# Kernel tuning notes

Hardware: AMD Instinct MI355X
Metric: run time of the kernel (lower is better)

## Reference

```python
import jax, jax.numpy as jnp
import numpy as np

N_UNI = 32; N_G = 4; N_PPG = 8
MAX_D = 100.0; MIN_D = 0.5
SOM_SIGMA = 2.0; G_STD = 2.5
ORIG = jnp.array([-25.6, -25.6, -2.0], jnp.float32); VS = 0.4
NZ = 16; GW = 128; GL = 128; DIM = 128
H_IMG = 352; W_IMG = 1216

def pe(x):
    # positional encoding: num_freqs=6, include_input -> 3 + 36 = 39 dims
    f = 2.0 ** jnp.arange(6, dtype=x.dtype)
    xf = x[..., None] * f  # (...,3,6)
    s = x.shape[:-1]
    return jnp.concatenate([x, jnp.sin(xf).reshape(s + (18,)), jnp.cos(xf).reshape(s + (18,))], axis=-1)

def resnet_fc(z, x, P):
    # pixelNeRF-style ResnetFC with latent injection per block
    w_in, b_in, wz, bz, w0, b0, w1, b1, w_out, b_out = P
    h = x @ w_in + b_in
    for i in range(3):
        h = h + z @ wz[i] + bz[i]
        net = jax.nn.relu(h) @ w0[i] + b0[i]
        h = h + jax.nn.relu(net) @ w1[i] + b1[i]
    return jax.nn.relu(h) @ w_out + b_out

def trilinear(grid, pts):
    # grid: (NZ,GW,GL,DIM); pts: (N,3) lidar coords -> trilinear gather, 0 outside
    g = (pts - ORIG) / VS
    gx, gy, gz = g[:, 0], g[:, 1], g[:, 2]
    inb = (gx >= 0) & (gx <= GW - 1) & (gy >= 0) & (gy <= GL - 1) & (gz >= 0) & (gz <= NZ - 1)
    gx = jnp.clip(gx, 0.0, GW - 1.0); gy = jnp.clip(gy, 0.0, GL - 1.0); gz = jnp.clip(gz, 0.0, NZ - 1.0)
    x0 = jnp.clip(jnp.floor(gx).astype(jnp.int32), 0, GW - 2)
    y0 = jnp.clip(jnp.floor(gy).astype(jnp.int32), 0, GL - 2)
    z0 = jnp.clip(jnp.floor(gz).astype(jnp.int32), 0, NZ - 2)
    fx = gx - x0; fy = gy - y0; fz = gz - z0
    def c(zi, xi, yi, w):
        return grid[zi, xi, yi] * w[:, None]
    feat = (c(z0, x0, y0, (1 - fz) * (1 - fx) * (1 - fy)) + c(z0, x0, y0 + 1, (1 - fz) * (1 - fx) * fy)
            + c(z0, x0 + 1, y0, (1 - fz) * fx * (1 - fy)) + c(z0, x0 + 1, y0 + 1, (1 - fz) * fx * fy)
            + c(z0 + 1, x0, y0, fz * (1 - fx) * (1 - fy)) + c(z0 + 1, x0, y0 + 1, fz * (1 - fx) * fy)
            + c(z0 + 1, x0 + 1, y0, fz * fx * (1 - fy)) + c(z0 + 1, x0 + 1, y0 + 1, fz * fx * fy))
    return feat * inb[:, None].astype(feat.dtype)

def bilinear(img, uv):
    # img: (3,H,W); uv: (N,2) (u=col, v=row) -> (N,3)
    _, H, W = img.shape
    u = jnp.clip(uv[:, 0], 0.0, W - 1.0); v = jnp.clip(uv[:, 1], 0.0, H - 1.0)
    u0 = jnp.clip(jnp.floor(u).astype(jnp.int32), 0, W - 2)
    v0 = jnp.clip(jnp.floor(v).astype(jnp.int32), 0, H - 2)
    fu = u - u0; fv = v - v0
    g = lambda vi, ui: img[:, vi, ui]
    out = (g(v0, u0) * ((1 - fv) * (1 - fu)) + g(v0, u0 + 1) * ((1 - fv) * fu)
           + g(v0 + 1, u0) * (fv * (1 - fu)) + g(v0 + 1, u0 + 1) * (fv * fu))
    return out.T

def _forward(bev_feature, cam_K, img_source, img_target, T_source2infer, T_source2target,
             gaussian_noise, Pm, Pg, sampled_pixels):
    R = sampled_pixels.shape[0]
    # (B, C, W, L) -> (n_z, W, L, dim)
    vf = bev_feature[0].reshape(NZ, DIM, GW, GL).transpose(0, 2, 3, 1)
    inv_K = jnp.linalg.inv(cam_K)
    pix = sampled_pixels.astype(jnp.float32)
    homog = jnp.concatenate([pix, jnp.ones((R, 1), jnp.float32)], axis=1)
    dirs = homog @ inv_K.T
    unit = dirs / jnp.linalg.norm(dirs, axis=1, keepdims=True)  # (R,3) cam frame
    Rsi = T_source2infer[:3, :3]; tsi = T_source2infer[:3, 3]
    viewdir = unit @ Rsi.T  # lidar frame

    # --- predict per-ray gaussian means/stds at coarse segment centers ---
    base = (jnp.arange(N_G, dtype=jnp.float32) + 0.5) * (MAX_D / N_G)
    pg = (unit[:, None, :] * base[None, :, None]).reshape(-1, 3) @ Rsi.T + tsi
    fg = trilinear(vf, pg)
    vdg = jnp.broadcast_to(viewdir[:, None, :], (R, N_G, 3)).reshape(-1, 3)
    og = resnet_fc(fg, jnp.concatenate([pe(pg), vdg], axis=1), Pg)  # (R*N_G,2)
    means = jnp.clip(base[None, :] + og[:, 0].reshape(R, N_G), MIN_D, MAX_D)
    stds = G_STD * jax.nn.sigmoid(og[:, 1].reshape(R, N_G)) + 0.1

    # --- sample points: uniform + gaussian, sorted along ray ---
    d_g = jnp.clip(means[:, :, None] + stds[:, :, None] * gaussian_noise, MIN_D, MAX_D).reshape(R, N_G * N_PPG)
    d_u = jnp.broadcast_to(jnp.linspace(MIN_D, MAX_D, N_UNI, dtype=jnp.float32)[None, :], (R, N_UNI))
    d = jnp.sort(jnp.concatenate([d_u, d_g], axis=1), axis=1)  # (R,64)
    P = d.shape[1]
    pl = (unit[:, None, :] * d[..., None]).reshape(-1, 3) @ Rsi.T + tsi
    fl = trilinear(vf, pl)
    vd = jnp.broadcast_to(viewdir[:, None, :], (R, P, 3)).reshape(-1, 3)
    out = resnet_fc(fl, jnp.concatenate([pe(pl), vd], axis=1), Pm).reshape(R, P, 4)
    sigma = jax.nn.softplus(out[..., 0]); rgb = jax.nn.sigmoid(out[..., 1:])

    # --- volume rendering ---
    deltas = jnp.concatenate([d[:, 1:] - d[:, :-1], jnp.full((R, 1), 1e10, jnp.float32)], axis=1)
    alpha = 1.0 - jnp.exp(-sigma * deltas)
    trans = jnp.cumprod(1.0 - alpha + 1e-10, axis=1)
    trans = jnp.concatenate([jnp.ones((R, 1), jnp.float32), trans[:, :-1]], axis=1)
    w = alpha * trans
    depth = (w * d).sum(axis=1)          # (R,)
    color = (w[..., None] * rgb).sum(axis=1)  # (R,3)

    # --- losses ---
    diff = jnp.abs(means - jax.lax.stop_gradient(depth)[:, None])
    loss_dist = diff.min(axis=1)
    pdf = jnp.exp(-(d[:, None, :] - means[..., None]) ** 2 / (2.0 * stds[..., None] ** 2)) / (stds[..., None] * jnp.sqrt(2.0 * jnp.pi))
    loss_kl = (w * (-jnp.log(pdf.mean(axis=1) + 1e-6))).sum(axis=1)
    src = bilinear(img_source, pix)
    loss_color = jnp.abs(src - color)
    pcam = unit * depth[:, None]
    pt = pcam @ T_source2target[:3, :3].T + T_source2target[:3, 3]
    proj = pt @ cam_K.T
    uv = proj[:, :2] / jnp.clip(proj[:, 2:3], 1e-3)
    tgt = bilinear(img_target, uv)
    loss_reproj = jnp.abs(src - tgt)
    total = loss_reproj.mean() + loss_color.mean() + loss_kl.mean() + 0.01 * loss_dist.mean()
    return total

def setup_inputs() -> dict:
    key = jax.random.key(0)
    def rn(i, shape, s=1.0):
        return jax.random.normal(jax.random.fold_in(key, i), shape, jnp.float32) * s
    R = 4096
    inp = {}
    inp['bev_feature'] = rn(0, (1, NZ * DIM, GW, GL), 0.5)
    inp['cam_K'] = jnp.array([[720.0, 0.0, 608.0], [0.0, 720.0, 176.0], [0.0, 0.0, 1.0]], jnp.float32)
    inp['img_source'] = jax.random.uniform(jax.random.fold_in(key, 1), (3, H_IMG, W_IMG), jnp.float32)
    inp['img_target'] = jax.random.uniform(jax.random.fold_in(key, 2), (3, H_IMG, W_IMG), jnp.float32)
    Rcl = jnp.array([[0.0, 0.0, 1.0], [-1.0, 0.0, 0.0], [0.0, -1.0, 0.0]], jnp.float32)  # cam->lidar axes
    inp['T_source2infer'] = jnp.eye(4, dtype=jnp.float32).at[:3, :3].set(Rcl).at[:3, 3].set(jnp.array([0.5, 0.2, 0.1], jnp.float32))
    inp['T_source2target'] = jnp.eye(4, dtype=jnp.float32).at[0, 3].set(0.8).at[1, 3].set(0.05)
    inp['gaussian_noise'] = rn(3, (R, N_G, N_PPG))
    u = jax.random.randint(jax.random.fold_in(key, 4), (R,), 0, W_IMG)
    v = jax.random.randint(jax.random.fold_in(key, 5), (R,), 0, H_IMG)
    inp['sampled_pixels'] = jnp.stack([u, v], axis=1).astype(jnp.int32)
    for pfx, (i0, d_out) in {'m': (10, 4), 'g': (40, 2)}.items():
        inp[pfx + '_w_in'] = rn(i0, (42, 128), 0.05)
        inp[pfx + '_b_in'] = jnp.zeros((128,), jnp.float32)
        inp[pfx + '_wz'] = rn(i0 + 1, (3, 128, 128), 0.05)
        inp[pfx + '_bz'] = jnp.zeros((3, 128), jnp.float32)
        inp[pfx + '_w0'] = rn(i0 + 2, (3, 128, 128), 0.05)
        inp[pfx + '_b0'] = jnp.zeros((3, 128), jnp.float32)
        inp[pfx + '_w1'] = rn(i0 + 3, (3, 128, 128), 0.05)
        inp[pfx + '_b1'] = jnp.zeros((3, 128), jnp.float32)
        inp[pfx + '_w_out'] = rn(i0 + 4, (128, d_out), 0.05)
        inp[pfx + '_b_out'] = jnp.zeros((d_out,), jnp.float32)
    return inp

def reference(bev_feature, cam_K, img_source, img_target, T_source2infer, T_source2target,
              gaussian_noise, sampled_pixels,
              m_w_in, m_b_in, m_wz, m_bz, m_w0, m_b0, m_w1, m_b1, m_w_out, m_b_out,
              g_w_in, g_b_in, g_wz, g_bz, g_w0, g_b0, g_w1, g_b1, g_w_out, g_b_out):
    Pm = (m_w_in, m_b_in, m_wz, m_bz, m_w0, m_b0, m_w1, m_b1, m_w_out, m_b_out)
    Pg = (g_w_in, g_b_in, g_wz, g_bz, g_w0, g_b0, g_w1, g_b1, g_w_out, g_b_out)
    return _forward(bev_feature, cam_K, img_source, img_target, T_source2infer, T_source2target,
                    gaussian_noise, Pm, Pg, sampled_pixels)
```

## Files before the change

kernel.cpp:

```cpp
#include <hip/hip_runtime.h>

typedef __attribute__((ext_vector_type(8))) short short8;
typedef __attribute__((ext_vector_type(4))) float f32x4;
typedef __attribute__((ext_vector_type(2))) float f32x2;
typedef __attribute__((ext_vector_type(2))) unsigned u32x2;
typedef unsigned short ushort_t;

#define WIMG 1216
#define HIMG 352

__device__ __forceinline__ float sigmoid_(float x){ return 1.f/(1.f+__expf(-x)); }
__device__ __forceinline__ float softplus_(float x){
  return fmaxf(x,0.f) + log1pf(__expf(-fabsf(x)));
}
__device__ __forceinline__ ushort_t f2b(float x){
  union { float f; unsigned u; } v; v.f = x;
  unsigned r = v.u + 0x7FFF + ((v.u >> 16) & 1);
  return (ushort_t)(r >> 16);
}
__device__ __forceinline__ unsigned pack_trunc(float a, float b){
  union { float f; unsigned u; } va, vb; va.f = a; vb.f = b;
  return (va.u >> 16) | (vb.u & 0xFFFF0000u);
}
__device__ __forceinline__ unsigned cvt_pk_bf16(float a, float b){
// ... 53 lines not shown
  const float* w0   = net ? gw0   : mw0;
  const float* w1   = net ? gw1   : mw1;
  const float* wo   = net ? gwo   : mwo;
  int outd = net ? 2 : 4;
  ushort_t* pk = net ? pkG : pkM;
  int id = (pb - (net ? 624 : 0))*256 + tid;
  if (id >= 39*4096) return;
  int blk = id >> 12;
  int e = id & 4095;
  float val = 0.f;
  if (blk < 38) {
    int nt = e >> 9, lane = (e >> 3) & 63, j = e & 7;
    int kloc = (lane >> 4)*8 + j;
    int n = nt*16 + (lane & 15);
    if (blk < 2) {
      int k = blk*32 + kloc;
      val = (k < 42) ? w_in[k*128 + n] : 0.f;
    } else {
      int g = blk - 2;
      int i = g / 12, r = g % 12, m = r >> 2, ks = r & 3;
      int k = ks*32 + kloc;
      const float* src = (m==0 ? wz : (m==1 ? w0 : w1)) + i*16384;
      val = src[k*128 + n];
    }
  } else if (e < 2048) {
    int ks = e >> 9, lane = (e >> 3) & 63, j = e & 7;
    int k = ks*32 + (lane >> 4)*8 + j;
    int n = lane & 15;
    val = (n < outd) ? wo[k*outd + n] : 0.f;
  }
  pk[id] = f2b(val);
}

template<int KS, bool SWZ>
__device__ __forceinline__ void gemm_frag(const ushort_t* lds,
                                          const ushort_t* __restrict__ pkW,
                                          f32x4 acc[2][4], int wave, int lane)
{
  short8 w[KS][2];
  #pragma unroll
  for (int ks = 0; ks < KS; ++ks)
    #pragma unroll
    for (int ct = 0; ct < 2; ++ct)
      w[ks][ct] = *(const short8*)(pkW + (size_t)((ks*8 + wave*2 + ct)*64 + lane)*8);
  #pragma unroll
  for (int ks = 0; ks < KS; ++ks) {
    int idx = SWZ ? ((lane & ~7) | ((lane ^ (lane >> 3) ^ ks) & 7)) : lane;
    short8 b[4];
    #pragma unroll
    for (int nt = 0; nt < 4; ++nt)
      b[nt] = *(const short8*)(lds + (ks*4 + nt)*512 + idx*8);
    __builtin_amdgcn_s_setprio(1);
    #pragma unroll
    for (int ct = 0; ct < 2; ++ct)
      #pragma unroll
      for (int nt = 0; nt < 4; ++nt)
        acc[ct][nt] = __builtin_amdgcn_mfma_f32_16x16x32_bf16(w[ks][ct], b[nt], acc[ct][nt], 0,0,0);
    __builtin_amdgcn_s_setprio(0);
  }
}

__device__ __forceinline__ void store_reluF(ushort_t* buf, const f32x4 acc[2][4],
                                            int wave, int lane){
  int l15 = lane & 15, quad = lane >> 4;
  int j = (quad & 1)*4;
  #pragma unroll
  for (int ct = 0; ct < 2; ++ct) {
    int lp = (ct*2 + (quad >> 1))*16 + l15;
    #pragma unroll
    for (int nt = 0; nt < 4; ++nt) {
      uint2 o;
      o.x = cvt_pk_bf16(fmaxf(acc[ct][nt][0],0.f), fmaxf(acc[ct][nt][1],0.f));
      o.y = cvt_pk_bf16(fmaxf(acc[ct][nt][2],0.f), fmaxf(acc[ct][nt][3],0.f));
      *(uint2*)(buf + (wave*4 + nt)*512 + lp*8 + j) = o;
    }
  }
}

template<int OUTD>
__global__ __launch_bounds__(256, 4)
void k_fused(const ushort_t* __restrict__ vfh, const float* __restrict__ vf0, int mode,
             const float* __restrict__ camK, const int* __restrict__ pix,
             const float* __restrict__ noise,
             float* __restrict__ unit, float* __restrict__ viewdir,
             const float* __restrict__ Tsi, float* __restrict__ dsort,
             const ushort_t* __restrict__ pk,
             const float* __restrict__ b_in, const float* __restrict__ bzv,
             const float* __restrict__ b0v, const float* __restrict__ b1v,
             const float* __restrict__ b_out,
             float* __restrict__ means, float* __restrict__ stds, float* __restrict__ outbuf)
{
  extern __shared__ __align__(16) ushort_t smem[];
  ushort_t* zf = smem;
  ushort_t* Wb = smem + 8192;
  float* auxf = (float*)Wb;
  int*   sOff = (int*)auxf;
  float (*sW)[8] = (float(*)[8])(auxf + 64);
  float* sPx = auxf + 576;
  float* sPy = auxf + 640;
  float* sPz = auxf + 704;
  float* sUx = auxf + 768; float* sUy = auxf + 784; float* sUz = auxf + 800;
  float* sVx = auxf + 816; float* sVy = auxf + 832; float* sVz = auxf + 848;
  float* zff = (float*)zf;
  float* sMean = zff + 3072;
  float* sStd  = zff + 3136;

  int tid = threadIdx.x;
  int qbase = blockIdx.x * 64;

  if constexpr (OUTD == 2) {
    if (tid < 16) {
      int gray = (qbase >> 2) + tid;
      float a=camK[0],b=camK[1],c=camK[2],d=camK[3],e=camK[4],f=camK[5],g=camK[6],h=camK[7],i=camK[8];
      float c00 = e*i-f*h, c01 = c*h-b*i, c02 = b*f-c*e;
      float c10 = f*g-d*i, c11 = a*i-c*g, c12 = c*d-a*f;
      float c20 = d*h-e*g, c21 = b*g-a*h, c22 = a*e-b*d;
      float det = a*c00 + b*c10 + c*c20;
      float id = 1.f/det;
      float u = (float)pix[2*gray], v = (float)pix[2*gray+1];
      float dx = (c00*u + c01*v + c02)*id;
      float dy = (c10*u + c11*v + c12)*id;
      float dz = (c20*u + c21*v + c22)*id;
      float n = sqrtf(dx*dx+dy*dy+dz*dz);
      dx/=n; dy/=n; dz/=n;
      sUx[tid]=dx; sUy[tid]=dy; sUz[tid]=dz;
      unit[3*gray]=dx; unit[3*gray+1]=dy; unit[3*gray+2]=dz;
      float vx = Tsi[0]*dx + Tsi[1]*dy + Tsi[2]*dz;
      float vy = Tsi[4]*dx + Tsi[5]*dy + Tsi[6]*dz;
      float vz = Tsi[8]*dx + Tsi[9]*dy + Tsi[10]*dz;
      sVx[tid]=vx; sVy[tid]=vy; sVz[tid]=vz;
      viewdir[3*gray]=vx; viewdir[3*gray+1]=vy; viewdir[3*gray+2]=vz;
    }
  } else {
    if (tid == 0) {
      int ray = blockIdx.x;
      sUx[0]=unit[3*ray]; sUy[0]=unit[3*ray+1]; sUz[0]=unit[3*ray+2];
      sVx[0]=viewdir[3*ray]; sVy[0]=viewdir[3*ray+1]; sVz[0]=viewdir[3*ray+2];
    }
  }
  __syncthreads();

  if (tid < 64) {
    float t, ux, uy, uz;
    if constexpr (OUTD == 2) {
      t = ((float)(tid & 3) + 0.5f) * 25.f;
      int lr = tid >> 2;
      ux = sUx[lr]; uy = sUy[lr]; uz = sUz[lr];
    } else {
      t = dsort[qbase + tid];
      ux = sUx[0]; uy = sUy[0]; uz = sUz[0];
    }
    float wx=ux*t, wy=uy*t, wz=uz*t;
    float px = Tsi[0]*wx + Tsi[1]*wy + Tsi[2]*wz + Tsi[3];
    float py = Tsi[4]*wx + Tsi[5]*wy + Tsi[6]*wz + Tsi[7];
    float pz = Tsi[8]*wx + Tsi[9]*wy + Tsi[10]*wz + Tsi[11];
    sPx[tid]=px; sPy[tid]=py; sPz[tid]=pz;
    float gx = (px + 25.6f)*2.5f;
    float gy = (py + 25.6f)*2.5f;
    float gz = (pz + 2.0f)*2.5f;
    bool inb = (gx>=0.f)&&(gx<=127.f)&&(gy>=0.f)&&(gy<=127.f)&&(gz>=0.f)&&(gz<=15.f);
    gx = fminf(fmaxf(gx,0.f),127.f);
    gy = fminf(fmaxf(gy,0.f),127.f);
    gz = fminf(fmaxf(gz,0.f),15.f);
    int x0 = min(max((int)floorf(gx),0),126);
    int y0 = min(max((int)floorf(gy),0),126);
    int z0 = min(max((int)floorf(gz),0),14);
    float fx = gx-(float)x0, fy = gy-(float)y0, fz = gz-(float)z0;
    float sc = inb ? 1.f : 0.f;
    float ax0 = 1.f-fx, ay0 = 1.f-fy;
    float az0 = (1.f-fz)*sc, az1 = fz*sc;
    float q00 = ax0*ay0, q01 = ax0*fy, q10 = fx*ay0, q11 = fx*fy;
    sW[tid][0] = az0*q00; sW[tid][1] = az0*q01; sW[tid][2] = az0*q10; sW[tid][3] = az0*q11;
    sW[tid][4] = az1*q00; sW[tid][5] = az1*q01; sW[tid][6] = az1*q10; sW[tid][7] = az1*q11;
    sOff[tid] = mode ? (((z0*128 + x0)*128 + y0)*128)
                     : (z0*2097152 + x0*128 + y0);
  }
  __syncthreads();

  for (int it = 0; it < 4; ++it) {
    int lin = it*256 + tid;
    int p = lin >> 4, cb = lin & 15;
    float4 wA = *(const float4*)&sW[p][0];
    float4 wB = *(const float4*)&sW[p][4];
    f32x2 r01={0.f,0.f}, r23={0.f,0.f}, r45={0.f,0.f}, r67={0.f,0.f};
    if (mode) {
      const ushort_t* b = vfh + sOff[p] + cb*8;
      uint4 v;
      #define ACC8(PTR, W) \
        v = *(const uint4*)(PTR); \
        r01 += (W)*bf2x(v.x); r23 += (W)*bf2x(v.y); \
        r45 += (W)*bf2x(v.z); r67 += (W)*bf2x(v.w);
      ACC8(b,                     wA.x)
      ACC8(b + 128,               wA.y)
      ACC8(b + 16384,             wA.z)
      ACC8(b + 16384 + 128,       wA.w)
      ACC8(b + 2097152,           wB.x)
      ACC8(b + 2097152 + 128,     wB.y)
      ACC8(b + 2097152 + 16384,   wB.z)
      ACC8(b + 2097152 + 16512,   wB.w)
      #undef ACC8
    } else {
      const float* bsrc = vf0 + sOff[p];
      float rr[8];
      #pragma unroll
      for (int k = 0; k < 8; ++k) {
        const float* bc = bsrc + (size_t)(cb*8 + k)*16384;
        rr[k] = wA.x*bc[0] + wA.y*bc[1] + wA.z*bc[128] + wA.w*bc[129]
              + wB.x*bc[2097152] + wB.y*bc[2097153] + wB.z*bc[2097280] + wB.w*bc[2097281];
      }
      r01 = (f32x2){rr[0],rr[1]}; r23 = (f32x2){rr[2],rr[3]};
      r45 = (f32x2){rr[4],rr[5]}; r67 = (f32x2){rr[6],rr[7]};
    }
    uint4 o;
    o.x = cvt_pk_bf16(r01.x, r01.y); o.y = cvt_pk_bf16(r23.x, r23.y);
    o.z = cvt_pk_bf16(r45.x, r45.y); o.w = cvt_pk_bf16(r67.x, r67.y);
    int T = (cb >> 2)*4 + (p >> 4);
    int lanep = (cb & 3)*16 + (p & 15);
    int lsw = (lanep & ~7) | ((lanep ^ (lanep >> 3) ^ (cb >> 2)) & 7);
    *(uint4*)(zf + T*512 + lsw*8) = o;
  }

  int pp = tid & 63;
  float ppx = sPx[pp], ppy = sPy[pp], ppz = sPz[pp];
  int plr = (OUTD == 2) ? (pp >> 2) : 0;
  float pvx = sVx[plr], pvy = sVy[plr], pvz = sVz[plr];
  __syncthreads();

  {
    int p = pp, wv = tid >> 6;
    #pragma unroll
    for (int hf = 0; hf < 2; ++hf) {
      int g = hf*4 + wv;
      float vals[8];
      #pragma unroll
      for (int j = 0; j < 8; ++j) {
        int d = g*8 + j;
        float val = 0.f;
        if (d < 3)      val = (d==0)?ppx:((d==1)?ppy:ppz);
        else if (d < 39) {
          int s = d - 3; bool isSin = (s < 18); if (!isSin) s -= 18;
          int axis = s/6, fi = s%6;
          float base = (axis==0)?ppx:((axis==1)?ppy:ppz);
          float arg = base * (float)(1 << fi);
          val = isSin ? __sinf(arg) : __cosf(arg);
        } else if (d < 42) {
          val = (d==39)?pvx:((d==40)?pvy:pvz);
        }
        vals[j] = val;
      }
      uint4 o;
      o.x = cvt_pk_bf16(vals[0], vals[1]);
      o.y = cvt_pk_bf16(vals[2], vals[3]);
      o.z = cvt_pk_bf16(vals[4], vals[5]);
      o.w = cvt_pk_bf16(vals[6], vals[7]);
      *(uint4*)(Wb + (g>>2)*2048 + (p>>4)*512 + ((g&3)*16 + (p&15))*8) = o;
    }
  }
  __syncthreads();

  int wave = tid >> 6, lane = tid & 63;
  int l15 = lane & 15, quad = lane >> 4;
  int cbase = wave*32 + quad*4;

  f32x4 h[2][4];
  #pragma unroll
  for (int ct = 0; ct < 2; ++ct) {
    f32x4 bi = *(const f32x4*)(b_in + cbase + ct*16);
    #pragma unroll
    for (int nt = 0; nt < 4; ++nt) h[ct][nt] = bi;
  }
  gemm_frag<2,false>(Wb, pk, h, wave, lane);

  const ushort_t* pkl = pk + 2*4096;
  #pragma unroll 1
  for (int i3 = 0; i3 < 3; ++i3) {
    gemm_frag<4,true>(zf, pkl + (size_t)(i3*12)*4096, h, wave, lane);
    #pragma unroll
    for (int ct = 0; ct < 2; ++ct) {
      f32x4 bz = *(const f32x4*)(bzv + i3*128 + cbase + ct*16);
      #pragma unroll
      for (int nt = 0; nt < 4; ++nt) h[ct][nt] += bz;
    }
    __syncthreads();
    store_reluF(Wb, h, wave, lane);
    __syncthreads();
    f32x4 net[2][4];
    #pragma unroll
    for (int ct = 0; ct < 2; ++ct) {
      f32x4 c0b = *(const f32x4*)(b0v + i3*128 + cbase + ct*16);
      #pragma unroll
      for (int nt = 0; nt < 4; ++nt) net[ct][nt] = c0b;
    }
    gemm_frag<4,false>(Wb, pkl + (size_t)(i3*12+4)*4096, net, wave, lane);
    __syncthreads();
    store_reluF(Wb, net, wave, lane);
    __syncthreads();
    gemm_frag<4,false>(Wb, pkl + (size_t)(i3*12+8)*4096, h, wave, lane);
    #pragma unroll
    for (int ct = 0; ct < 2; ++ct) {
      f32x4 o1b = *(const f32x4*)(b1v + i3*128 + cbase + ct*16);
      #pragma unroll
      for (int nt = 0; nt < 4; ++nt) h[ct][nt] += o1b;
    }
  }
  __syncthreads();
  store_reluF(Wb, h, wave, lane);
  __syncthreads();

  {
    const ushort_t* pkw = pk + 38*4096;
    f32x4 oa = (f32x4){0.f,0.f,0.f,0.f};
    #pragma unroll
    for (int ks = 0; ks < 4; ++ks) {
      short8 w = *(const short8*)(pkw + (size_t)(ks*64 + lane)*8);
      short8 b = *(const short8*)(Wb + (ks*4 + wave)*512 + lane*8);
      oa = __builtin_amdgcn_mfma_f32_16x16x32_bf16(w, b, oa, 0,0,0);
    }
    if (quad == 0) {
      int lq = wave*16 + l15;
      int q = qbase + lq;
      if constexpr (OUTD == 4) {
        float4 o = { oa[0] + b_out[0], oa[1] + b_out[1], oa[2] + b_out[2], oa[3] + b_out[3] };
        *(float4*)(outbuf + (size_t)q*4) = o;
      } else {
        int g = q & 3;
        float m = fminf(fmaxf(((float)g + 0.5f)*25.f + oa[0] + b_out[0], 0.5f), 100.f);
        float sd = 2.5f*sigmoid_(oa[1] + b_out[1]) + 0.1f;
        means[q] = m; stds[q] = sd;
        sMean[lq] = m; sStd[lq] = sd;
      }
    }
  }

  if constexpr (OUTD == 2) {
    __syncthreads();
    float* fbuf = zff;
    int lr = tid >> 4;
    int sbase = (tid & 15) * 4;
    float vals[4];
    #pragma unroll
    for (int s = 0; s < 4; ++s) {
      int slot = sbase + s;
      float val;
      if (slot < 32) val = 0.5f + (float)slot * (99.5f/31.f);
      else {
        int idx = slot - 32, g = idx >> 3, sx = idx & 7;
        int lq = lr*4 + g;
        float mu = sMean[lq], sd = sStd[lq];
        val = fminf(fmaxf(mu + sd*noise[(size_t)(qbase + lq)*8 + sx], 0.5f), 100.f);
      }
      fbuf[lr*64 + slot] = val;
      vals[s] = val;
    }
    __syncthreads();
    int rk[4] = {0,0,0,0};
    for (int k = 0; k < 64; ++k) {
      float o = fbuf[lr*64 + k];
      #pragma unroll
      for (int s = 0; s < 4; ++s)
        rk[s] += (o < vals[s]) || (o == vals[s] && k < sbase + s);
    }
    int gray = (qbase >> 2) + lr;
    #pragma unroll
    for (int s = 0; s < 4; ++s)
      dsort[(size_t)gray*64 + rk[s]] = vals[s];
  }
}

__device__ __forceinline__ void bilin3(const float* __restrict__ img, float u, float v, float* out){
  u = fminf(fmaxf(u, 0.f), (float)(WIMG-1));
  v = fminf(fmaxf(v, 0.f), (float)(HIMG-1));
  int u0 = min(max((int)floorf(u),0), WIMG-2);
  int v0 = min(max((int)floorf(v),0), HIMG-2);
  float fu = u - (float)u0, fv = v - (float)v0;
  float w00=(1.f-fv)*(1.f-fu), w01=(1.f-fv)*fu, w10=fv*(1.f-fu), w11=fv*fu;
  #pragma unroll
  for (int c = 0; c < 3; ++c) {
    const float* b = img + (size_t)c*(HIMG*WIMG) + (size_t)v0*WIMG + u0;
    out[c] = w00*b[0] + w01*b[1] + w10*b[WIMG] + w11*b[WIMG+1];
  }
}

__global__ void k_render(const float* __restrict__ outbuf, const float* __restrict__ dsort,
                         const float* __restrict__ means, const float* __restrict__ stds,
                         const float* __restrict__ unit,
                         const float* __restrict__ img_src, const float* __restrict__ img_tgt,
                         const int* __restrict__ pix, const float* __restrict__ camK,
                         const float* __restrict__ Tst, float* __restrict__ loss_out, int R){
  __shared__ float accw[4];
  int gid = blockIdx.x*blockDim.x + threadIdx.x;
  int r = gid >> 6, lane = gid & 63;
  float d = dsort[(size_t)r*64 + lane];
  float dn = __shfl_down(d, 1);
  float delta = (lane < 63) ? (dn - d) : 1e10f;
  float4 o = *(const float4*)(outbuf + (size_t)r*256 + lane*4);
  float sig = softplus_(o.x);
  float alpha = 1.f - __expf(-sig*delta);
  float om = 1.f - alpha + 1e-10f;
// ... 62 lines not shown
  const float* noise = (const float*)d_in[6];
  const int*   pix   = (const int*)d_in[7];
  const float* m_w_in=(const float*)d_in[8];  const float* m_b_in=(const float*)d_in[9];
  const float* m_wz  =(const float*)d_in[10]; const float* m_bz  =(const float*)d_in[11];
  const float* m_w0  =(const float*)d_in[12]; const float* m_b0  =(const float*)d_in[13];
  const float* m_w1  =(const float*)d_in[14]; const float* m_b1  =(const float*)d_in[15];
  const float* m_wo  =(const float*)d_in[16]; const float* m_bo  =(const float*)d_in[17];
  const float* g_w_in=(const float*)d_in[18]; const float* g_b_in=(const float*)d_in[19];
  const float* g_wz  =(const float*)d_in[20]; const float* g_bz  =(const float*)d_in[21];
  const float* g_w0  =(const float*)d_in[22]; const float* g_b0  =(const float*)d_in[23];
  const float* g_w1  =(const float*)d_in[24]; const float* g_b1  =(const float*)d_in[25];
  const float* g_wo  =(const float*)d_in[26]; const float* g_bo  =(const float*)d_in[27];

  int R = in_sizes[7] / 2;
  float* ws = (float*)d_ws;
  size_t off = 0;
  float* unitb = ws + off; off += (size_t)R*3;
  float* vdirb = ws + off; off += (size_t)R*3;
  float* means = ws + off; off += (size_t)R*4;
  float* stds  = ws + off; off += (size_t)R*4;
  float* dsort = ws + off; off += (size_t)R*64;
  float* outbf = ws + off; off += (size_t)R*256;
  ushort_t* pkM = (ushort_t*)(ws + off);
  ushort_t* pkG = pkM + 39*4096;
  off += 39*4096 + 64;
  off = (off + 63) & ~(size_t)63;
  ushort_t* vfh = (ushort_t*)(ws + off);
  size_t need = off*4ull + (size_t)16*128*128*128*2ull;
  int mode = (ws_size >= need) ? 1 : 0;

  k_prep<<<9440,256,0,stream>>>(bev, vfh, mode,
      m_w_in,m_wz,m_w0,m_w1,m_wo, g_w_in,g_wz,g_w0,g_w1,g_wo,
      pkM, pkG, (float*)d_out);
  k_fused<2><<<R/16,256, 32768, stream>>>(vfh,bev,mode,camK,pix,noise,unitb,vdirb,Tsi,dsort,pkG,
      g_b_in,g_bz,g_b0,g_b1,g_bo, means,stds,nullptr);
  k_fused<4><<<R,256, 32768, stream>>>(vfh,bev,mode,camK,pix,noise,unitb,vdirb,Tsi,dsort,pkM,
      m_b_in,m_bz,m_b0,m_b1,m_bo, means,stds,outbf);
  k_render<<<R/4,256,0,stream>>>(outbf,dsort,means,stds,unitb,img_s,img_t,pix,camK,Tst,
                                 (float*)d_out,R);
}
```

Before: 432.9 us.

## Prefetch next GEMM weight fragments into registers across MLP layers

Measured after the change: 500.3 us. 15.6% more time.

```diff
diff --git a/kernel.cpp b/kernel.cpp
--- a/kernel.cpp
+++ b/kernel.cpp
@@ -109,17 +109,31 @@
   pk[id] = f2b(val);
 }
 
+struct WPre { short8 a[2][2]; };
+
+__device__ __forceinline__ void load_pre(WPre& W, const ushort_t* __restrict__ pkW,
+                                         int wave, int lane){
+  #pragma unroll
+  for (int ks = 0; ks < 2; ++ks)
+    #pragma unroll
+    for (int ct = 0; ct < 2; ++ct)
+      W.a[ks][ct] = *(const short8*)(pkW + (size_t)((ks*8 + wave*2 + ct)*64 + lane)*8);
+}
+
 template<int KS, bool SWZ>
-__device__ __forceinline__ void gemm_frag(const ushort_t* lds,
-                                          const ushort_t* __restrict__ pkW,
-                                          f32x4 acc[2][4], int wave, int lane)
+__device__ __forceinline__ void gemm_pre(const ushort_t* lds,
+                                         const ushort_t* __restrict__ pkW,
+                                         const WPre& W,
+                                         f32x4 acc[2][4], int wave, int lane)
 {
-  short8 w[KS][2];
-  #pragma unroll
-  for (int ks = 0; ks < KS; ++ks)
-    #pragma unroll
-    for (int ct = 0; ct < 2; ++ct)
-      w[ks][ct] = *(const short8*)(pkW + (size_t)((ks*8 + wave*2 + ct)*64 + lane)*8);
+  short8 wl[2][2];
+  if constexpr (KS == 4) {
+    #pragma unroll
+    for (int ks = 2; ks < 4; ++ks)
+      #pragma unroll
+      for (int ct = 0; ct < 2; ++ct)
+        wl[ks-2][ct] = *(const short8*)(pkW + (size_t)((ks*8 + wave*2 + ct)*64 + lane)*8);
+  }
   #pragma unroll
   for (int ks = 0; ks < KS; ++ks) {
     int idx = SWZ ? ((lane & ~7) | ((lane ^ (lane >> 3) ^ ks) & 7)) : lane;
@@ -127,12 +141,15 @@
     #pragma unroll
     for (int nt = 0; nt < 4; ++nt)
       b[nt] = *(const short8*)(lds + (ks*4 + nt)*512 + idx*8);
+    short8 w0s = (ks < 2) ? W.a[ks & 1][0] : wl[ks & 1][0];
+    short8 w1s = (ks < 2) ? W.a[ks & 1][1] : wl[ks & 1][1];
     __builtin_amdgcn_s_setprio(1);
     #pragma unroll
-    for (int ct = 0; ct < 2; ++ct)
-      #pragma unroll
-      for (int nt = 0; nt < 4; ++nt)
-        acc[ct][nt] = __builtin_amdgcn_mfma_f32_16x16x32_bf16(w[ks][ct], b[nt], acc[ct][nt], 0,0,0);
+    for (int nt = 0; nt < 4; ++nt)
+      acc[0][nt] = __builtin_amdgcn_mfma_f32_16x16x32_bf16(w0s, b[nt], acc[0][nt], 0,0,0);
+    #pragma unroll
+    for (int nt = 0; nt < 4; ++nt)
+      acc[1][nt] = __builtin_amdgcn_mfma_f32_16x16x32_bf16(w1s, b[nt], acc[1][nt], 0,0,0);
     __builtin_amdgcn_s_setprio(0);
   }
 }
@@ -167,7 +184,7 @@
              const float* __restrict__ b_out,
              float* __restrict__ means, float* __restrict__ stds, float* __restrict__ outbuf)
 {
-  extern __shared__ __align__(16) ushort_t smem[];
+  __shared__ __align__(16) ushort_t smem[16384];
   ushort_t* zf = smem;
   ushort_t* Wb = smem + 8192;
   float* auxf = (float*)Wb;
@@ -183,6 +200,7 @@
   float* sStd  = zff + 3136;
 
   int tid = threadIdx.x;
+  int wave = tid >> 6, lane = tid & 63;
   int qbase = blockIdx.x * 64;
 
   if constexpr (OUTD == 2) {
@@ -297,6 +315,9 @@
     *(uint4*)(zf + T*512 + lsw*8) = o;
   }
 
+  WPre Win; load_pre(Win, pk, wave, lane);
+  WPre Wz;  load_pre(Wz,  pk + 2*4096, wave, lane);
+
   int pp = tid & 63;
   float ppx = sPx[pp], ppy = sPy[pp], ppz = sPz[pp];
   int plr = (OUTD == 2) ? (pp >> 2) : 0;
@@ -335,7 +356,6 @@
   }
   __syncthreads();
 
-  int wave = tid >> 6, lane = tid & 63;
   int l15 = lane & 15, quad = lane >> 4;
   int cbase = wave*32 + quad*4;
 
@@ -346,12 +366,17 @@
     #pragma unroll
     for (int nt = 0; nt < 4; ++nt) h[ct][nt] = bi;
   }
-  gemm_frag<2,false>(Wb, pk, h, wave, lane);
+  gemm_pre<2,false>(Wb, pk, Win, h, wave, lane);
 
   const ushort_t* pkl = pk + 2*4096;
+  WPre Wn;
   #pragma unroll 1
   for (int i3 = 0; i3 < 3; ++i3) {
-    gemm_frag<4,true>(zf, pkl + (size_t)(i3*12)*4096, h, wave, lane);
+    const ushort_t* pz = pkl + (size_t)(i3*12)*4096;
+    const ushort_t* p0 = pkl + (size_t)(i3*12+4)*4096;
+    const ushort_t* p1 = pkl + (size_t)(i3*12+8)*4096;
+    load_pre(Wn, p0, wave, lane);
+    gemm_pre<4,true>(zf, pz, Wz, h, wave, lane);
     #pragma unroll
     for (int ct = 0; ct < 2; ++ct) {
       f32x4 bz = *(const f32x4*)(bzv + i3*128 + cbase + ct*16);
@@ -361,6 +386,7 @@
     __syncthreads();
     store_reluF(Wb, h, wave, lane);
     __syncthreads();
+    load_pre(Wz, p1, wave, lane);
     f32x4 net[2][4];
     #pragma unroll
     for (int ct = 0; ct < 2; ++ct) {
@@ -368,30 +394,37 @@
       #pragma unroll
       for (int nt = 0; nt < 4; ++nt) net[ct][nt] = c0b;
     }
-    gemm_frag<4,false>(Wb, pkl + (size_t)(i3*12+4)*4096, net, wave, lane);
+    gemm_pre<4,false>(Wb, p0, Wn, net, wave, lane);
     __syncthreads();
     store_reluF(Wb, net, wave, lane);
     __syncthreads();
-    gemm_frag<4,false>(Wb, pkl + (size_t)(i3*12+8)*4096, h, wave, lane);
+    load_pre(Wn, pkl + (size_t)(((i3+1)%3)*12)*4096, wave, lane);
+    gemm_pre<4,false>(Wb, p1, Wz, h, wave, lane);
     #pragma unroll
     for (int ct = 0; ct < 2; ++ct) {
       f32x4 o1b = *(const f32x4*)(b1v + i3*128 + cbase + ct*16);
       #pragma unroll
       for (int nt = 0; nt < 4; ++nt) h[ct][nt] += o1b;
     }
-  }
+    Wz = Wn;
+  }
+
+  const ushort_t* pkw = pk + 38*4096;
+  short8 we[4];
+  #pragma unroll
+  for (int ks = 0; ks < 4; ++ks)
+    we[ks] = *(const short8*)(pkw + (size_t)(ks*64 + lane)*8);
+
   __syncthreads();
   store_reluF(Wb, h, wave, lane);
   __syncthreads();
 
   {
-    const ushort_t* pkw = pk + 38*4096;
     f32x4 oa = (f32x4){0.f,0.f,0.f,0.f};
     #pragma unroll
     for (int ks = 0; ks < 4; ++ks) {
-      short8 w = *(const short8*)(pkw + (size_t)(ks*64 + lane)*8);
       short8 b = *(const short8*)(Wb + (ks*4 + wave)*512 + lane*8);
-      oa = __builtin_amdgcn_mfma_f32_16x16x32_bf16(w, b, oa, 0,0,0);
+      oa = __builtin_amdgcn_mfma_f32_16x16x32_bf16(we[ks], b, oa, 0,0,0);
     }
     if (quad == 0) {
       int lq = wave*16 + l15;
@@ -569,9 +602,9 @@
   k_prep<<<9440,256,0,stream>>>(bev, vfh, mode,
       m_w_in,m_wz,m_w0,m_w1,m_wo, g_w_in,g_wz,g_w0,g_w1,g_wo,
       pkM, pkG, (float*)d_out);
-  k_fused<2><<<R/16,256, 32768, stream>>>(vfh,bev,mode,camK,pix,noise,unitb,vdirb,Tsi,dsort,pkG,
+  k_fused<2><<<R/16,256,0,stream>>>(vfh,bev,mode,camK,pix,noise,unitb,vdirb,Tsi,dsort,pkG,
       g_b_in,g_bz,g_b0,g_b1,g_bo, means,stds,nullptr);
-  k_fused<4><<<R,256, 32768, stream>>>(vfh,bev,mode,camK,pix,noise,unitb,vdirb,Tsi,dsort,pkM,
+  k_fused<4><<<R,256,0,stream>>>(vfh,bev,mode,camK,pix,noise,unitb,vdirb,Tsi,dsort,pkM,
       m_b_in,m_bz,m_b0,m_b1,m_bo, means,stds,outbf);
   k_render<<<R/4,256,0,stream>>>(outbf,dsort,means,stds,unitb,img_s,img_t,pix,camK,Tst,
                                  (float*)d_out,R);
```

## Split fused MLP across 8 waves with per-wave point and channel groups

Applied to the files above, without the earlier changes.

New measurement: 645.5 us. +49.1%, slower.

```diff
diff --git a/kernel.cpp b/kernel.cpp
--- a/kernel.cpp
+++ b/kernel.cpp
@@ -112,50 +112,50 @@
 template<int KS, bool SWZ>
 __device__ __forceinline__ void gemm_frag(const ushort_t* lds,
                                           const ushort_t* __restrict__ pkW,
-                                          f32x4 acc[2][4], int wave, int lane)
+                                          f32x4 acc[2][2], int cg, int pg, int lane)
 {
   short8 w[KS][2];
   #pragma unroll
   for (int ks = 0; ks < KS; ++ks)
     #pragma unroll
     for (int ct = 0; ct < 2; ++ct)
-      w[ks][ct] = *(const short8*)(pkW + (size_t)((ks*8 + wave*2 + ct)*64 + lane)*8);
+      w[ks][ct] = *(const short8*)(pkW + (size_t)((ks*8 + cg*2 + ct)*64 + lane)*8);
   #pragma unroll
   for (int ks = 0; ks < KS; ++ks) {
     int idx = SWZ ? ((lane & ~7) | ((lane ^ (lane >> 3) ^ ks) & 7)) : lane;
-    short8 b[4];
-    #pragma unroll
-    for (int nt = 0; nt < 4; ++nt)
-      b[nt] = *(const short8*)(lds + (ks*4 + nt)*512 + idx*8);
+    short8 b[2];
+    #pragma unroll
+    for (int nt = 0; nt < 2; ++nt)
+      b[nt] = *(const short8*)(lds + (ks*4 + pg*2 + nt)*512 + idx*8);
     __builtin_amdgcn_s_setprio(1);
     #pragma unroll
     for (int ct = 0; ct < 2; ++ct)
       #pragma unroll
-      for (int nt = 0; nt < 4; ++nt)
+      for (int nt = 0; nt < 2; ++nt)
         acc[ct][nt] = __builtin_amdgcn_mfma_f32_16x16x32_bf16(w[ks][ct], b[nt], acc[ct][nt], 0,0,0);
     __builtin_amdgcn_s_setprio(0);
   }
 }
 
-__device__ __forceinline__ void store_reluF(ushort_t* buf, const f32x4 acc[2][4],
-                                            int wave, int lane){
+__device__ __forceinline__ void store_reluF(ushort_t* buf, const f32x4 acc[2][2],
+                                            int cg, int pg, int lane){
   int l15 = lane & 15, quad = lane >> 4;
   int j = (quad & 1)*4;
   #pragma unroll
   for (int ct = 0; ct < 2; ++ct) {
     int lp = (ct*2 + (quad >> 1))*16 + l15;
     #pragma unroll
-    for (int nt = 0; nt < 4; ++nt) {
+    for (int nt = 0; nt < 2; ++nt) {
       uint2 o;
       o.x = cvt_pk_bf16(fmaxf(acc[ct][nt][0],0.f), fmaxf(acc[ct][nt][1],0.f));
       o.y = cvt_pk_bf16(fmaxf(acc[ct][nt][2],0.f), fmaxf(acc[ct][nt][3],0.f));
-      *(uint2*)(buf + (wave*4 + nt)*512 + lp*8 + j) = o;
+      *(uint2*)(buf + (cg*4 + pg*2 + nt)*512 + lp*8 + j) = o;
     }
   }
 }
 
 template<int OUTD>
-__global__ __launch_bounds__(256, 4)
+__global__ __launch_bounds__(512, 8)
 void k_fused(const ushort_t* __restrict__ vfh, const float* __restrict__ vf0, int mode,
              const float* __restrict__ camK, const int* __restrict__ pix,
              const float* __restrict__ noise,
@@ -167,7 +167,7 @@
              const float* __restrict__ b_out,
              float* __restrict__ means, float* __restrict__ stds, float* __restrict__ outbuf)
 {
-  extern __shared__ __align__(16) ushort_t smem[];
+  __shared__ __align__(16) ushort_t smem[16384];
   ushort_t* zf = smem;
   ushort_t* Wb = smem + 8192;
   float* auxf = (float*)Wb;
@@ -183,6 +183,8 @@
   float* sStd  = zff + 3136;
 
   int tid = threadIdx.x;
+  int wv = tid >> 6, lane = tid & 63;
+  int cg = wv & 3, pg = wv >> 2;
   int qbase = blockIdx.x * 64;
 
   if constexpr (OUTD == 2) {
@@ -254,8 +256,8 @@
   }
   __syncthreads();
 
-  for (int it = 0; it < 4; ++it) {
-    int lin = it*256 + tid;
+  for (int it = 0; it < 2; ++it) {
+    int lin = it*512 + tid;
     int p = lin >> 4, cb = lin & 15;
     float4 wA = *(const float4*)&sW[p][0];
     float4 wB = *(const float4*)&sW[p][4];
@@ -297,104 +299,99 @@
     *(uint4*)(zf + T*512 + lsw*8) = o;
   }
 
-  int pp = tid & 63;
+  int pp = lane;
   float ppx = sPx[pp], ppy = sPy[pp], ppz = sPz[pp];
   int plr = (OUTD == 2) ? (pp >> 2) : 0;
   float pvx = sVx[plr], pvy = sVy[plr], pvz = sVz[plr];
   __syncthreads();
 
   {
-    int p = pp, wv = tid >> 6;
-    #pragma unroll
-    for (int hf = 0; hf < 2; ++hf) {
-      int g = hf*4 + wv;
-      float vals[8];
-      #pragma unroll
-      for (int j = 0; j < 8; ++j) {
-        int d = g*8 + j;
-        float val = 0.f;
-        if (d < 3)      val = (d==0)?ppx:((d==1)?ppy:ppz);
-        else if (d < 39) {
-          int s = d - 3; bool isSin = (s < 18); if (!isSin) s -= 18;
-          int axis = s/6, fi = s%6;
-          float base = (axis==0)?ppx:((axis==1)?ppy:ppz);
-          float arg = base * (float)(1 << fi);
-          val = isSin ? __sinf(arg) : __cosf(arg);
-        } else if (d < 42) {
-          val = (d==39)?pvx:((d==40)?pvy:pvz);
-        }
-        vals[j] = val;
+    int p = pp, g = wv;
+    float vals[8];
+    #pragma unroll
+    for (int j = 0; j < 8; ++j) {
+      int d = g*8 + j;
+      float val = 0.f;
+      if (d < 3)      val = (d==0)?ppx:((d==1)?ppy:ppz);
+      else if (d < 39) {
+        int s = d - 3; bool isSin = (s < 18); if (!isSin) s -= 18;
+        int axis = s/6, fi = s%6;
+        float base = (axis==0)?ppx:((axis==1)?ppy:ppz);
+        float arg = base * (float)(1 << fi);
+        val = isSin ? __sinf(arg) : __cosf(arg);
+      } else if (d < 42) {
+        val = (d==39)?pvx:((d==40)?pvy:pvz);
       }
-      uint4 o;
-      o.x = cvt_pk_bf16(vals[0], vals[1]);
-      o.y = cvt_pk_bf16(vals[2], vals[3]);
-      o.z = cvt_pk_bf16(vals[4], vals[5]);
-      o.w = cvt_pk_bf16(vals[6], vals[7]);
-      *(uint4*)(Wb + (g>>2)*2048 + (p>>4)*512 + ((g&3)*16 + (p&15))*8) = o;
-    }
-  }
-  __syncthreads();
-
-  int wave = tid >> 6, lane = tid & 63;
+      vals[j] = val;
+    }
+    uint4 o;
+    o.x = cvt_pk_bf16(vals[0], vals[1]);
+    o.y = cvt_pk_bf16(vals[2], vals[3]);
+    o.z = cvt_pk_bf16(vals[4], vals[5]);
+    o.w = cvt_pk_bf16(vals[6], vals[7]);
+    *(uint4*)(Wb + (g>>2)*2048 + (p>>4)*512 + ((g&3)*16 + (p&15))*8) = o;
+  }
+  __syncthreads();
+
   int l15 = lane & 15, quad = lane >> 4;
-  int cbase = wave*32 + quad*4;
-
-  f32x4 h[2][4];
+  int cbase = cg*32 + quad*4;
+
+  f32x4 h[2][2];
   #pragma unroll
   for (int ct = 0; ct < 2; ++ct) {
     f32x4 bi = *(const f32x4*)(b_in + cbase + ct*16);
     #pragma unroll
-    for (int nt = 0; nt < 4; ++nt) h[ct][nt] = bi;
-  }
-  gemm_frag<2,false>(Wb, pk, h, wave, lane);
+    for (int nt = 0; nt < 2; ++nt) h[ct][nt] = bi;
+  }
+  gemm_frag<2,false>(Wb, pk, h, cg, pg, lane);
 
   const ushort_t* pkl = pk + 2*4096;
   #pragma unroll 1
   for (int i3 = 0; i3 < 3; ++i3) {
-    gemm_frag<4,true>(zf, pkl + (size_t)(i3*12)*4096, h, wave, lane);
+    gemm_frag<4,true>(zf, pkl + (size_t)(i3*12)*4096, h, cg, pg, lane);
     #pragma unroll
     for (int ct = 0; ct < 2; ++ct) {
       f32x4 bz = *(const f32x4*)(bzv + i3*128 + cbase + ct*16);
       #pragma unroll
-      for (int nt = 0; nt < 4; ++nt) h[ct][nt] += bz;
-    }
-    __syncthreads();
-    store_reluF(Wb, h, wave, lane);
-    __syncthreads();
-    f32x4 net[2][4];
+      for (int nt = 0; nt < 2; ++nt) h[ct][nt] += bz;
+    }
+    __syncthreads();
+    store_reluF(Wb, h, cg, pg, lane);
+    __syncthreads();
+    f32x4 net[2][2];
     #pragma unroll
     for (int ct = 0; ct < 2; ++ct) {
       f32x4 c0b = *(const f32x4*)(b0v + i3*128 + cbase + ct*16);
       #pragma unroll
-      for (int nt = 0; nt < 4; ++nt) net[ct][nt] = c0b;
-    }
-    gemm_frag<4,false>(Wb, pkl + (size_t)(i3*12+4)*4096, net, wave, lane);
-    __syncthreads();
-    store_reluF(Wb, net, wave, lane);
-    __syncthreads();
-    gemm_frag<4,false>(Wb, pkl + (size_t)(i3*12+8)*4096, h, wave, lane);
+      for (int nt = 0; nt < 2; ++nt) net[ct][nt] = c0b;
+    }
+    gemm_frag<4,false>(Wb, pkl + (size_t)(i3*12+4)*4096, net, cg, pg, lane);
+    __syncthreads();
+    store_reluF(Wb, net, cg, pg, lane);
+    __syncthreads();
+    gemm_frag<4,false>(Wb, pkl + (size_t)(i3*12+8)*4096, h, cg, pg, lane);
     #pragma unroll
     for (int ct = 0; ct < 2; ++ct) {
       f32x4 o1b = *(const f32x4*)(b1v + i3*128 + cbase + ct*16);
       #pragma unroll
-      for (int nt = 0; nt < 4; ++nt) h[ct][nt] += o1b;
-    }
-  }
-  __syncthreads();
-  store_reluF(Wb, h, wave, lane);
-  __syncthreads();
-
-  {
+      for (int nt = 0; nt < 2; ++nt) h[ct][nt] += o1b;
+    }
+  }
+  __syncthreads();
+  store_reluF(Wb, h, cg, pg, lane);
+  __syncthreads();
+
+  if (wv < 4) {
     const ushort_t* pkw = pk + 38*4096;
     f32x4 oa = (f32x4){0.f,0.f,0.f,0.f};
     #pragma unroll
     for (int ks = 0; ks < 4; ++ks) {
       short8 w = *(const short8*)(pkw + (size_t)(ks*64 + lane)*8);
-      short8 b = *(const short8*)(Wb + (ks*4 + wave)*512 + lane*8);
+      short8 b = *(const short8*)(Wb + (ks*4 + wv)*512 + lane*8);
       oa = __builtin_amdgcn_mfma_f32_16x16x32_bf16(w, b, oa, 0,0,0);
     }
     if (quad == 0) {
-      int lq = wave*16 + l15;
+      int lq = wv*16 + l15;
       int q = qbase + lq;
       if constexpr (OUTD == 4) {
         float4 o = { oa[0] + b_out[0], oa[1] + b_out[1], oa[2] + b_out[2], oa[3] + b_out[3] };
@@ -415,32 +412,36 @@
     int lr = tid >> 4;
     int sbase = (tid & 15) * 4;
     float vals[4];
-    #pragma unroll
-    for (int s = 0; s < 4; ++s) {
-      int slot = sbase + s;
-      float val;
-      if (slot < 32) val = 0.5f + (float)slot * (99.5f/31.f);
-      else {
-        int idx = slot - 32, g = idx >> 3, sx = idx & 7;
-        int lq = lr*4 + g;
-        float mu = sMean[lq], sd = sStd[lq];
-        val = fminf(fmaxf(mu + sd*noise[(size_t)(qbase + lq)*8 + sx], 0.5f), 100.f);
+    if (tid < 256) {
+      #pragma unroll
+      for (int s = 0; s < 4; ++s) {
+        int slot = sbase + s;
+        float val;
+        if (slot < 32) val = 0.5f + (float)slot * (99.5f/31.f);
+        else {
+          int idx = slot - 32, g = idx >> 3, sx = idx & 7;
+          int lq = lr*4 + g;
+          float mu = sMean[lq], sd = sStd[lq];
+          val = fminf(fmaxf(mu + sd*noise[(size_t)(qbase + lq)*8 + sx], 0.5f), 100.f);
+        }
+        fbuf[lr*64 + slot] = val;
+        vals[s] = val;
       }
-      fbuf[lr*64 + slot] = val;
-      vals[s] = val;
-    }
-    __syncthreads();
-    int rk[4] = {0,0,0,0};
-    for (int k = 0; k < 64; ++k) {
-      float o = fbuf[lr*64 + k];
+    }
+    __syncthreads();
+    if (tid < 256) {
+      int rk[4] = {0,0,0,0};
+      for (int k = 0; k < 64; ++k) {
+        float o = fbuf[lr*64 + k];
+        #pragma unroll
+        for (int s = 0; s < 4; ++s)
+          rk[s] += (o < vals[s]) || (o == vals[s] && k < sbase + s);
+      }
+      int gray = (qbase >> 2) + lr;
       #pragma unroll
       for (int s = 0; s < 4; ++s)
-        rk[s] += (o < vals[s]) || (o == vals[s] && k < sbase + s);
-    }
-    int gray = (qbase >> 2) + lr;
-    #pragma unroll
-    for (int s = 0; s < 4; ++s)
-      dsort[(size_t)gray*64 + rk[s]] = vals[s];
+        dsort[(size_t)gray*64 + rk[s]] = vals[s];
+    }
   }
 }
 
@@ -569,9 +570,9 @@
   k_prep<<<9440,256,0,stream>>>(bev, vfh, mode,
       m_w_in,m_wz,m_w0,m_w1,m_wo, g_w_in,g_wz,g_w0,g_w1,g_wo,
       pkM, pkG, (float*)d_out);
-  k_fused<2><<<R/16,256, 32768, stream>>>(vfh,bev,mode,camK,pix,noise,unitb,vdirb,Tsi,dsort,pkG,
+  k_fused<2><<<R/16,512,0,stream>>>(vfh,bev,mode,camK,pix,noise,unitb,vdirb,Tsi,dsort,pkG,
       g_b_in,g_bz,g_b0,g_b1,g_bo, means,stds,nullptr);
-  k_fused<4><<<R,256, 32768, stream>>>(vfh,bev,mode,camK,pix,noise,unitb,vdirb,Tsi,dsort,pkM,
+  k_fused<4><<<R,512,0,stream>>>(vfh,bev,mode,camK,pix,noise,unitb,vdirb,Tsi,dsort,pkM,
       m_b_in,m_bz,m_b0,m_b1,m_bo, means,stds,outbf);
   k_render<<<R/4,256,0,stream>>>(outbf,dsort,means,stds,unitb,img_s,img_t,pix,camK,Tst,
                                  (float*)d_out,R);
```

## Double fused MLP block to 128 points with 512 threads across two point groups

Applied to the files above, without the earlier changes.

Measured after the change: 415.0 us. 4.1% less time.

```diff
diff --git a/kernel.cpp b/kernel.cpp
--- a/kernel.cpp
+++ b/kernel.cpp
@@ -112,21 +112,21 @@
 template<int KS, bool SWZ>
 __device__ __forceinline__ void gemm_frag(const ushort_t* lds,
                                           const ushort_t* __restrict__ pkW,
-                                          f32x4 acc[2][4], int wave, int lane)
+                                          f32x4 acc[2][4], int cg, int pg, int lane)
 {
   short8 w[KS][2];
   #pragma unroll
   for (int ks = 0; ks < KS; ++ks)
     #pragma unroll
     for (int ct = 0; ct < 2; ++ct)
-      w[ks][ct] = *(const short8*)(pkW + (size_t)((ks*8 + wave*2 + ct)*64 + lane)*8);
+      w[ks][ct] = *(const short8*)(pkW + (size_t)((ks*8 + cg*2 + ct)*64 + lane)*8);
   #pragma unroll
   for (int ks = 0; ks < KS; ++ks) {
     int idx = SWZ ? ((lane & ~7) | ((lane ^ (lane >> 3) ^ ks) & 7)) : lane;
     short8 b[4];
     #pragma unroll
     for (int nt = 0; nt < 4; ++nt)
-      b[nt] = *(const short8*)(lds + (ks*4 + nt)*512 + idx*8);
+      b[nt] = *(const short8*)(lds + (ks*8 + pg*4 + nt)*512 + idx*8);
     __builtin_amdgcn_s_setprio(1);
     #pragma unroll
     for (int ct = 0; ct < 2; ++ct)
@@ -138,7 +138,7 @@
 }
 
 __device__ __forceinline__ void store_reluF(ushort_t* buf, const f32x4 acc[2][4],
-                                            int wave, int lane){
+                                            int cg, int pg, int lane){
   int l15 = lane & 15, quad = lane >> 4;
   int j = (quad & 1)*4;
   #pragma unroll
@@ -149,13 +149,13 @@
       uint2 o;
       o.x = cvt_pk_bf16(fmaxf(acc[ct][nt][0],0.f), fmaxf(acc[ct][nt][1],0.f));
       o.y = cvt_pk_bf16(fmaxf(acc[ct][nt][2],0.f), fmaxf(acc[ct][nt][3],0.f));
-      *(uint2*)(buf + (wave*4 + nt)*512 + lp*8 + j) = o;
+      *(uint2*)(buf + (cg*8 + pg*4 + nt)*512 + lp*8 + j) = o;
     }
   }
 }
 
 template<int OUTD>
-__global__ __launch_bounds__(256, 4)
+__global__ __launch_bounds__(512, 4)
 void k_fused(const ushort_t* __restrict__ vfh, const float* __restrict__ vf0, int mode,
              const float* __restrict__ camK, const int* __restrict__ pix,
              const float* __restrict__ noise,
@@ -167,26 +167,28 @@
              const float* __restrict__ b_out,
              float* __restrict__ means, float* __restrict__ stds, float* __restrict__ outbuf)
 {
-  extern __shared__ __align__(16) ushort_t smem[];
+  __shared__ __align__(16) ushort_t smem[32768];
   ushort_t* zf = smem;
-  ushort_t* Wb = smem + 8192;
+  ushort_t* Wb = smem + 16384;
   float* auxf = (float*)Wb;
   int*   sOff = (int*)auxf;
-  float (*sW)[8] = (float(*)[8])(auxf + 64);
-  float* sPx = auxf + 576;
-  float* sPy = auxf + 640;
-  float* sPz = auxf + 704;
-  float* sUx = auxf + 768; float* sUy = auxf + 784; float* sUz = auxf + 800;
-  float* sVx = auxf + 816; float* sVy = auxf + 832; float* sVz = auxf + 848;
+  float (*sW)[8] = (float(*)[8])(auxf + 128);
+  float* sPx = auxf + 1152;
+  float* sPy = auxf + 1280;
+  float* sPz = auxf + 1408;
+  float* sUx = auxf + 1536; float* sUy = auxf + 1568; float* sUz = auxf + 1600;
+  float* sVx = auxf + 1632; float* sVy = auxf + 1664; float* sVz = auxf + 1696;
   float* zff = (float*)zf;
-  float* sMean = zff + 3072;
-  float* sStd  = zff + 3136;
+  float* sMean = zff + 2048;
+  float* sStd  = zff + 2176;
 
   int tid = threadIdx.x;
-  int qbase = blockIdx.x * 64;
+  int wv = tid >> 6, lane = tid & 63;
+  int cg = wv & 3, pg = wv >> 2;
+  int qbase = blockIdx.x * 128;
 
   if constexpr (OUTD == 2) {
-    if (tid < 16) {
+    if (tid < 32) {
       int gray = (qbase >> 2) + tid;
       float a=camK[0],b=camK[1],c=camK[2],d=camK[3],e=camK[4],f=camK[5],g=camK[6],h=camK[7],i=camK[8];
       float c00 = e*i-f*h, c01 = c*h-b*i, c02 = b*f-c*e;
@@ -209,15 +211,15 @@
       viewdir[3*gray]=vx; viewdir[3*gray+1]=vy; viewdir[3*gray+2]=vz;
     }
   } else {
-    if (tid == 0) {
-      int ray = blockIdx.x;
-      sUx[0]=unit[3*ray]; sUy[0]=unit[3*ray+1]; sUz[0]=unit[3*ray+2];
-      sVx[0]=viewdir[3*ray]; sVy[0]=viewdir[3*ray+1]; sVz[0]=viewdir[3*ray+2];
-    }
-  }
-  __syncthreads();
-
-  if (tid < 64) {
+    if (tid < 2) {
+      int ray = blockIdx.x*2 + tid;
+      sUx[tid]=unit[3*ray]; sUy[tid]=unit[3*ray+1]; sUz[tid]=unit[3*ray+2];
+      sVx[tid]=viewdir[3*ray]; sVy[tid]=viewdir[3*ray+1]; sVz[tid]=viewdir[3*ray+2];
+    }
+  }
+  __syncthreads();
+
+  if (tid < 128) {
     float t, ux, uy, uz;
     if constexpr (OUTD == 2) {
       t = ((float)(tid & 3) + 0.5f) * 25.f;
@@ -225,7 +227,8 @@
       ux = sUx[lr]; uy = sUy[lr]; uz = sUz[lr];
     } else {
       t = dsort[qbase + tid];
-      ux = sUx[0]; uy = sUy[0]; uz = sUz[0];
+      int lr = tid >> 6;
+      ux = sUx[lr]; uy = sUy[lr]; uz = sUz[lr];
     }
     float wx=ux*t, wy=uy*t, wz=uz*t;
     float px = Tsi[0]*wx + Tsi[1]*wy + Tsi[2]*wz + Tsi[3];
@@ -255,7 +258,7 @@
   __syncthreads();
 
   for (int it = 0; it < 4; ++it) {
-    int lin = it*256 + tid;
+    int lin = it*512 + tid;
     int p = lin >> 4, cb = lin & 15;
     float4 wA = *(const float4*)&sW[p][0];
     float4 wB = *(const float4*)&sW[p][4];
@@ -291,23 +294,23 @@
     uint4 o;
     o.x = cvt_pk_bf16(r01.x, r01.y); o.y = cvt_pk_bf16(r23.x, r23.y);
     o.z = cvt_pk_bf16(r45.x, r45.y); o.w = cvt_pk_bf16(r67.x, r67.y);
-    int T = (cb >> 2)*4 + (p >> 4);
+    int T = (cb >> 2)*8 + (p >> 4);
     int lanep = (cb & 3)*16 + (p & 15);
     int lsw = (lanep & ~7) | ((lanep ^ (lanep >> 3) ^ (cb >> 2)) & 7);
     *(uint4*)(zf + T*512 + lsw*8) = o;
   }
 
-  int pp = tid & 63;
+  int pp = tid & 127;
   float ppx = sPx[pp], ppy = sPy[pp], ppz = sPz[pp];
-  int plr = (OUTD == 2) ? (pp >> 2) : 0;
+  int plr = (OUTD == 2) ? (pp >> 2) : (pp >> 6);
   float pvx = sVx[plr], pvy = sVy[plr], pvz = sVz[plr];
   __syncthreads();
 
   {
-    int p = pp, wv = tid >> 6;
+    int p = pp, wv2 = tid >> 7;
     #pragma unroll
     for (int hf = 0; hf < 2; ++hf) {
-      int g = hf*4 + wv;
+      int g = hf*4 + wv2;
       float vals[8];
       #pragma unroll
       for (int j = 0; j < 8; ++j) {
@@ -330,14 +333,13 @@
       o.y = cvt_pk_bf16(vals[2], vals[3]);
       o.z = cvt_pk_bf16(vals[4], vals[5]);
       o.w = cvt_pk_bf16(vals[6], vals[7]);
-      *(uint4*)(Wb + (g>>2)*2048 + (p>>4)*512 + ((g&3)*16 + (p&15))*8) = o;
-    }
-  }
-  __syncthreads();
-
-  int wave = tid >> 6, lane = tid & 63;
+      *(uint4*)(Wb + ((g>>2)*8 + (p>>4))*512 + (((g&3)*16 + (p&15)))*8) = o;
+    }
+  }
+  __syncthreads();
+
   int l15 = lane & 15, quad = lane >> 4;
-  int cbase = wave*32 + quad*4;
+  int cbase = cg*32 + quad*4;
 
   f32x4 h[2][4];
   #pragma unroll
@@ -346,12 +348,12 @@
     #pragma unroll
     for (int nt = 0; nt < 4; ++nt) h[ct][nt] = bi;
   }
-  gemm_frag<2,false>(Wb, pk, h, wave, lane);
+  gemm_frag<2,false>(Wb, pk, h, cg, pg, lane);
 
   const ushort_t* pkl = pk + 2*4096;
   #pragma unroll 1
   for (int i3 = 0; i3 < 3; ++i3) {
-    gemm_frag<4,true>(zf, pkl + (size_t)(i3*12)*4096, h, wave, lane);
+    gemm_frag<4,true>(zf, pkl + (size_t)(i3*12)*4096, h, cg, pg, lane);
     #pragma unroll
     for (int ct = 0; ct < 2; ++ct) {
       f32x4 bz = *(const f32x4*)(bzv + i3*128 + cbase + ct*16);
@@ -359,7 +361,7 @@
       for (int nt = 0; nt < 4; ++nt) h[ct][nt] += bz;
     }
     __syncthreads();
-    store_reluF(Wb, h, wave, lane);
+    store_reluF(Wb, h, cg, pg, lane);
     __syncthreads();
     f32x4 net[2][4];
     #pragma unroll
@@ -368,11 +370,11 @@
       #pragma unroll
       for (int nt = 0; nt < 4; ++nt) net[ct][nt] = c0b;
     }
-    gemm_frag<4,false>(Wb, pkl + (size_t)(i3*12+4)*4096, net, wave, lane);
-    __syncthreads();
-    store_reluF(Wb, net, wave, lane);
-    __syncthreads();
-    gemm_frag<4,false>(Wb, pkl + (size_t)(i3*12+8)*4096, h, wave, lane);
+    gemm_frag<4,false>(Wb, pkl + (size_t)(i3*12+4)*4096, net, cg, pg, lane);
+    __syncthreads();
+    store_reluF(Wb, net, cg, pg, lane);
+    __syncthreads();
+    gemm_frag<4,false>(Wb, pkl + (size_t)(i3*12+8)*4096, h, cg, pg, lane);
     #pragma unroll
     for (int ct = 0; ct < 2; ++ct) {
       f32x4 o1b = *(const f32x4*)(b1v + i3*128 + cbase + ct*16);
@@ -381,7 +383,7 @@
     }
   }
   __syncthreads();
-  store_reluF(Wb, h, wave, lane);
+  store_reluF(Wb, h, cg, pg, lane);
   __syncthreads();
 
   {
@@ -390,11 +392,11 @@
     #pragma unroll
     for (int ks = 0; ks < 4; ++ks) {
       short8 w = *(const short8*)(pkw + (size_t)(ks*64 + lane)*8);
-      short8 b = *(const short8*)(Wb + (ks*4 + wave)*512 + lane*8);
+      short8 b = *(const short8*)(Wb + (ks*8 + wv)*512 + lane*8);
       oa = __builtin_amdgcn_mfma_f32_16x16x32_bf16(w, b, oa, 0,0,0);
     }
     if (quad == 0) {
-      int lq = wave*16 + l15;
+      int lq = wv*16 + l15;
       int q = qbase + lq;
       if constexpr (OUTD == 4) {
         float4 o = { oa[0] + b_out[0], oa[1] + b_out[1], oa[2] + b_out[2], oa[3] + b_out[3] };
@@ -569,9 +571,9 @@
   k_prep<<<9440,256,0,stream>>>(bev, vfh, mode,
       m_w_in,m_wz,m_w0,m_w1,m_wo, g_w_in,g_wz,g_w0,g_w1,g_wo,
       pkM, pkG, (float*)d_out);
-  k_fused<2><<<R/16,256, 32768, stream>>>(vfh,bev,mode,camK,pix,noise,unitb,vdirb,Tsi,dsort,pkG,
+  k_fused<2><<<R/32,512,0,stream>>>(vfh,bev,mode,camK,pix,noise,unitb,vdirb,Tsi,dsort,pkG,
       g_b_in,g_bz,g_b0,g_b1,g_bo, means,stds,nullptr);
-  k_fused<4><<<R,256, 32768, stream>>>(vfh,bev,mode,camK,pix,noise,unitb,vdirb,Tsi,dsort,pkM,
+  k_fused<4><<<R/2,512,0,stream>>>(vfh,bev,mode,camK,pix,noise,unitb,vdirb,Tsi,dsort,pkM,
       m_b_in,m_bz,m_b0,m_b1,m_bo, means,stds,outbf);
   k_render<<<R/4,256,0,stream>>>(outbf,dsort,means,stds,unitb,img_s,img_t,pix,camK,Tst,
                                  (float*)d_out,R);
```
